# Optimization experiments

Hardware: AMD Instinct MI355X
Metric: run time of the kernel (lower is better)

Reference implementation:

```python
import jax, jax.numpy as jnp
import numpy as np
jax.config.update("jax_enable_x64", True)  # RWKV6 uses fp64 intra-chunk decay when chunk_len > 24

B, T, D, H = 2, 2048, 2048, 32
K = D // H
CHUNK = 128
EPS = 1e-5 * 8 ** 2  # GroupNorm eps * head_size_divisor**2


def setup_inputs() -> dict:
    ks = jax.random.split(jax.random.key(0), 24)
    f32 = jnp.float32
    s = 1.0 / np.sqrt(D).astype(np.float32)
    u = lambda k, sh, lo, hi: jax.random.uniform(k, sh, f32, lo, hi)
    n = lambda k, sh, sc=1.0: jax.random.normal(k, sh, f32) * sc
    return {
        "x": n(ks[0], (B, T, D)),
        "shift_state": n(ks[1], (B, D)),
        "wkv_state": jnp.zeros((B, H, K, K), f32),
        "time_maa_x": u(ks[2], (1, 1, D), 0.0, 1.0),
        "time_maa_w": u(ks[3], (1, 1, D), 0.0, 1.0),
        "time_maa_k": u(ks[4], (1, 1, D), 0.0, 1.0),
        "time_maa_v": u(ks[5], (1, 1, D), 0.0, 1.0),
        "time_maa_r": u(ks[6], (1, 1, D), 0.0, 1.0),
        "time_maa_g": u(ks[7], (1, 1, D), 0.0, 1.0),
        "time_maa_w1": n(ks[8], (D, 32 * 5), 0.01),
        "time_maa_w2": u(ks[9], (5, 32, D), -0.01, 0.01),
        "time_decay": u(ks[10], (1, 1, D), -6.0, -1.0),
        "time_decay_w1": n(ks[11], (D, 64), 0.1),
        "time_decay_w2": u(ks[12], (64, D), -0.01, 0.01),
        "time_faaaa": u(ks[13], (H, K), -0.1, 1.0),
        "W_r": n(ks[14], (D, D), s),
        "W_k": n(ks[15], (D, D), s),
        "W_v": n(ks[16], (D, D), s),
        "W_g": n(ks[17], (D, D), s),
        "W_o": n(ks[18], (D, D), s),
        "ln_gamma": jnp.ones((D,), f32),
        "ln_beta": jnp.zeros((D,), f32),
    }


def _wkv_chunked(r, k, v, w, u, state):
    """RWKV6 WKV: parallel intra-chunk (chunk_len=128, fp64 decay) + scan over chunks."""
    Bq, Hq, L, Kq = r.shape
    Tc = CHUNK
    N = L // Tc
    w_decay = jnp.clip(jnp.exp(w), 0.005, None)
    w_log = jnp.log(w_decay.astype(jnp.float32))
    wc_log = w_log.reshape(Bq, Hq, N, Tc, Kq)
    wc_cum = jnp.cumsum(wc_log, axis=-2)                               # (B,H,N,T,K)
    shifted = jnp.pad(wc_cum, ((0, 0),) * 3 + ((1, 0), (0, 0)))[..., :Tc, :]
    ws = jnp.sum(wc_log, axis=-2, keepdims=True)                        # (B,H,N,1,K)
    w_inter = jnp.exp(ws - wc_cum).astype(r.dtype)
    w_intra = jnp.exp(wc_cum - wc_log).astype(r.dtype)
    rc = r.reshape(Bq, Hq, N, Tc, Kq)
    kc = k.reshape(Bq, Hq, N, Tc, Kq)
    vc = v.reshape(Bq, Hq, N, Tc, Kq)
    off = shifted[..., Tc // 2:Tc // 2 + 1, :]
    r_decay = jnp.exp((shifted - off).astype(jnp.float64))
    k_inv = jnp.exp((off - wc_cum).astype(jnp.float64))
    a = jnp.einsum('bhnik,bhnjk->bhnij', rc * r_decay, kc * k_inv).astype(r.dtype)
    a = jnp.tril(a, -1)
    diag = jnp.einsum('bhntk,bhntk->bhnt', rc, u[:, :, None] * kc)      # u bonus on diagonal
    a = a + diag[..., None] * jnp.eye(Tc, dtype=a.dtype)
    out = jnp.einsum('bhnij,bhnjv->bhniv', a, vc)
    wkv = jnp.einsum('bhntk,bhntv->bhnkv', kc * w_inter, vc)
    ws_e = jnp.exp(ws)[..., 0, :, None].astype(r.dtype)                 # (B,H,N,K,1)

    def step(s, xs):
        wkv_i, ws_i = xs
        return s * ws_i + wkv_i, s  # emit state BEFORE update

    final, states = jax.lax.scan(step, state, (jnp.moveaxis(wkv, 2, 0), jnp.moveaxis(ws_e, 2, 0)))
    states = jnp.moveaxis(states, 0, 2)                                 # (B,H,N,K,V)
    out = out + jnp.einsum('bhntk,bhnkv->bhntv', rc * w_intra, states)
    return out.reshape(Bq, Hq, L, Kq), final


def _group_norm(x, n_groups, gamma, beta, eps):
    Bq, Tq, Dq = x.shape
    xg = x.reshape(Bq, Tq, n_groups, Dq // n_groups)
    mu = jnp.mean(xg, axis=-1, keepdims=True)
    var = jnp.var(xg, axis=-1, keepdims=True)
    xn = ((xg - mu) / jnp.sqrt(var + eps)).reshape(Bq, Tq, Dq)
    return xn * gamma + beta


def reference(x, shift_state, wkv_state, time_maa_x, time_maa_w, time_maa_k, time_maa_v,
              time_maa_r, time_maa_g, time_maa_w1, time_maa_w2, time_decay, time_decay_w1,
              time_decay_w2, time_faaaa, W_r, W_k, W_v, W_g, W_o, ln_gamma, ln_beta):
    Bq, Tq, Dq = x.shape
    Hq = time_faaaa.shape[0]
    Kq = Dq // Hq
    dxprev = jnp.concatenate([shift_state[:, None], x[:, :-1]], axis=1) - x
    xxx = x + dxprev * time_maa_x
    m = jnp.tanh(xxx @ time_maa_w1).reshape(Bq, Tq, 5, -1)
    m = jnp.einsum('btfm,fmd->fbtd', m, time_maa_w2)
    mw, mk, mv, mr, mg = m[0], m[1], m[2], m[3], m[4]
    xw = x + dxprev * (time_maa_w + mw)
    xk = x + dxprev * (time_maa_k + mk)
    xv = x + dxprev * (time_maa_v + mv)
    xr = x + dxprev * (time_maa_r + mr)
    xg = x + dxprev * (time_maa_g + mg)
    r = xr @ W_r.T
    k = xk @ W_k.T
    v = xv @ W_v.T
    g = jax.nn.silu(xg @ W_g.T)
    w = time_decay + jnp.tanh(xw @ time_decay_w1) @ time_decay_w2
    heads = lambda t: t.reshape(Bq, Tq, Hq, Kq).transpose(0, 2, 1, 3)
    r, k, v = heads(r), heads(k), heads(v)
    w = -jnp.exp(heads(w))
    u = time_faaaa.reshape(1, Hq, 1, Kq)
    x_out, wkv_out = _wkv_chunked(r, k, v, w, u, wkv_state)
    x_out = x_out.transpose(0, 2, 1, 3).reshape(Bq, Tq, Dq)
    x_out = _group_norm(x_out, Hq, ln_gamma, ln_beta, EPS)
    out = (x_out * g) @ W_o.T
    return out, x[:, -1], wkv_out
```

## Files before the change

kernel.cpp:

```cpp
#include <hip/hip_runtime.h>

#define B_ 2
#define T_ 2048
#define D_ 2048
#define H_ 32
#define BT_ 4096
#define TC 128

typedef unsigned short u16;
typedef unsigned int u32;
typedef __attribute__((ext_vector_type(8))) short short8;
typedef __attribute__((ext_vector_type(4))) float floatx4;

__device__ __forceinline__ float bf2f(u16 u){ return __uint_as_float(((u32)u)<<16); }
__device__ __forceinline__ u16 f2bf(float f){
  u32 i = __float_as_uint(f);
  if ((i & 0x7F800000u) == 0x7F800000u) return 0;
  return (u16)((i + 0x7FFFu + ((i>>16)&1u)) >> 16);
}
__device__ __forceinline__ float ldf(const void* p, int f, size_t i){
  return f ? ((const float*)p)[i] : bf2f(((const u16*)p)[i]);
}
__device__ __forceinline__ void async16(const u16* g, u16* l){
  __builtin_amdgcn_global_load_lds((const __attribute__((address_space(1))) void*)g,
                                   (__attribute__((address_space(3))) void*)l, 16, 0, 0);
}
__device__ __forceinline__ float sexp(float x){ return expf(fminf(x, 85.f)); }

#define LN005 -5.2983173665480363f

struct DetArgs { const void* p[22]; int n[22]; };

__global__ void k_detect(DetArgs a, int* fl){
  int t = threadIdx.x;
  if (t < 22){
    int bad = 0;
    if (t == 20){
      u32 w = *(const u32*)a.p[t];
      bad = (w == 0x3F800000u) ? 1 : 0;
    } else {
      int n = a.n[t];
      int step = n/256; if (step < 1) step = 1;
      const u16* u = (const u16*)a.p[t];
      for (int s=0; s<128; ++s){
        int j = (s*step) & ~1;
        if (j < n){
          u32 e = ((u32)u[j] >> 7) & 0xFFu;
          if (e >= 0xC0u) bad = 1;
        }
      }
    }
    fl[t] = bad;
  }
  __syncthreads();
  if (t == 0) fl[22] = fl[0];
}

__global__ void k_zero(u16* o, int n){
  int i = blockIdx.x*256 + threadIdx.x;
  if (i < n) o[i] = 0;
}

__global__ void k_wcvt(const void* __restrict__ src, const int* __restrict__ fl, int fidx,
                       u16* __restrict__ dst)
{
  if (!fl[fidx]) return;
  size_t i = ((size_t)blockIdx.x*256 + threadIdx.x)*8;
  const float* s = (const float*)src + i;
  float4 a0 = *(const float4*)s, a1 = *(const float4*)(s+4);
  u16 t[8] = {f2bf(a0.x),f2bf(a0.y),f2bf(a0.z),f2bf(a0.w),
              f2bf(a1.x),f2bf(a1.y),f2bf(a1.z),f2bf(a1.w)};
  *(uint4*)(dst + i) = *(uint4*)t;
}

__global__ void k_wtrans(const void* __restrict__ src, const int* __restrict__ fl, int fidx,
                         int K, int Nsrc, u16* __restrict__ dst)
{
  int f = fl[fidx];
  int kg = K >> 3;
  int i = blockIdx.x*256 + threadIdx.x;
  int n = i / kg, k0 = (i - n*kg) << 3;
  u16 tmp[8];
  if (n < Nsrc){
    if (f){
      const float* s = (const float*)src;
      #pragma unroll
      for (int j=0;j<8;++j) tmp[j] = f2bf(s[(size_t)(k0+j)*Nsrc + n]);
    } else {
      const u16* s = (const u16*)src;
      #pragma unroll
      for (int j=0;j<8;++j) tmp[j] = s[(size_t)(k0+j)*Nsrc + n];
    }
  } else {
    #pragma unroll
    for (int j=0;j<8;++j) tmp[j] = 0;
  }
  *(uint4*)(dst + (size_t)i*8) = *(uint4*)tmp;
}

__global__ void k_prep(const void* __restrict__ x, const void* __restrict__ shift,
                       const void* __restrict__ maax, const int* __restrict__ fl,
                       u16* __restrict__ dxp, u16* __restrict__ xxx)
{
  int xF = fl[0], sF = fl[1], mF = fl[3];
  int row = blockIdx.x;
  int t = row & (T_-1); int b = row >> 11;
  int d = threadIdx.x*8;
  size_t e = (size_t)row*D_ + d;
  float xf[8], pf[8], mf[8];
  if (xF){
    const float* xp = (const float*)x;
    float4 a0 = *(const float4*)(xp+e), a1 = *(const float4*)(xp+e+4);
    xf[0]=a0.x;xf[1]=a0.y;xf[2]=a0.z;xf[3]=a0.w;xf[4]=a1.x;xf[5]=a1.y;xf[6]=a1.z;xf[7]=a1.w;
    if (t>0){
      float4 p0 = *(const float4*)(xp+e-D_), p1 = *(const float4*)(xp+e-D_+4);
      pf[0]=p0.x;pf[1]=p0.y;pf[2]=p0.z;pf[3]=p0.w;pf[4]=p1.x;pf[5]=p1.y;pf[6]=p1.z;pf[7]=p1.w;
    } else {
      #pragma unroll
      for (int j=0;j<8;++j) pf[j] = ldf(shift, sF, (size_t)b*D_ + d + j);
    }
  } else {
    const u16* xp = (const u16*)x;
    u16 tmp[8];
    *(uint4*)tmp = *(const uint4*)(xp+e);
    #pragma unroll
    for (int j=0;j<8;++j) xf[j]=bf2f(tmp[j]);
    if (t>0){
      *(uint4*)tmp = *(const uint4*)(xp+e-D_);
      #pragma unroll
      for (int j=0;j<8;++j) pf[j]=bf2f(tmp[j]);
    } else {
      #pragma unroll
      for (int j=0;j<8;++j) pf[j] = ldf(shift, sF, (size_t)b*D_ + d + j);
    }
  }
  if (mF){
    const float* mp = (const float*)maax;
    float4 m0 = *(const float4*)(mp+d), m1 = *(const float4*)(mp+d+4);
    mf[0]=m0.x;mf[1]=m0.y;mf[2]=m0.z;mf[3]=m0.w;mf[4]=m1.x;mf[5]=m1.y;mf[6]=m1.z;mf[7]=m1.w;
  } else {
    #pragma unroll
    for (int j=0;j<8;++j) mf[j] = bf2f(((const u16*)maax)[d+j]);
  }
  u16 od[8], ox[8];
  #pragma unroll
  for (int j=0;j<8;++j){
    float dx = pf[j]-xf[j];
    od[j]=f2bf(dx);
    ox[j]=f2bf(xf[j]+dx*mf[j]);
  }
  *(uint4*)(dxp+e) = *(uint4*)od;
  *(uint4*)(xxx+e) = *(uint4*)ox;
}

#define EPI_BF16 0
#define EPI_OUT  1
#define EPI_TANH 2
#define EPI_WLOG 3
#define EPI_V    4
__global__ __launch_bounds__(256) void k_gemm(
    const u16* __restrict__ A, const void* __restrict__ Bsrc, const u16* __restrict__ Bcvt,
    void* __restrict__ Cv,
    int N, int K, int lda, int ldb,
    const int* __restrict__ fl, int bFlagIdx, int epi,
    const void* __restrict__ bias, int biasFlagIdx)
{
  __shared__ u16 As[128*64];
  __shared__ u16 Bs[128*64];
  const u16* Bp = ((bFlagIdx >= 0) && fl[bFlagIdx]) ? Bcvt : (const u16*)Bsrc;
  int tid = threadIdx.x;
  int wave = tid>>6, lane = tid&63;
  int q = lane>>4, l15 = lane&15;
  int row0 = blockIdx.x*128, col0 = blockIdx.y*128;
  int wm = (wave&1)*64, wn = (wave>>1)*64;
  floatx4 acc[4][4];
  #pragma unroll
  for (int i=0;i<4;++i)
    #pragma unroll
    for (int j=0;j<4;++j) acc[i][j] = (floatx4){0.f,0.f,0.f,0.f};

  for (int k0=0;k0<K;k0+=64){
    #pragma unroll
    for (int r=0;r<4;++r){
      int s = r*256 + tid;
      int row = s>>3, c8 = s&7;
      async16(A  + (size_t)(row0+row)*lda + k0 + c8*8, &As[s*8]);
      async16(Bp + (size_t)(col0+row)*ldb + k0 + c8*8, &Bs[s*8]);
    }
    __syncthreads();
    #pragma unroll
    for (int ks=0;ks<2;++ks){
      short8 af[4], bfv[4];
      #pragma unroll
      for (int i=0;i<4;++i){
        af[i]  = *(const short8*)&As[(wm + i*16 + l15)*64 + (ks*4+q)*8];
        bfv[i] = *(const short8*)&Bs[(wn + i*16 + l15)*64 + (ks*4+q)*8];
      }
      #pragma unroll
      for (int i=0;i<4;++i)
        #pragma unroll
        for (int j=0;j<4;++j)
          acc[i][j] = __builtin_amdgcn_mfma_f32_16x16x32_bf16(af[i], bfv[j], acc[i][j], 0,0,0);
    }
    __syncthreads();
  }
  if (epi == EPI_V){
    #pragma unroll
    for (int i=0;i<4;++i)
      #pragma unroll
      for (int j=0;j<4;++j){
        int row = row0 + wm + i*16 + q*4;
        int col = col0 + wn + j*16 + l15;
        int bb = row>>11, ta = row&2047;
        int nn = ta>>7, tt = ta&127;
        int h2 = col>>6, dim = col&63;
        u16 pk[4];
        #pragma unroll
        for (int rr=0;rr<4;++rr) pk[rr] = f2bf(acc[i][j][rr]);
        size_t vidx = ((size_t)(bb*H_+h2)*16+nn)*8192 + (size_t)dim*128 + tt;
        *(uint2*)((u16*)Cv + vidx) = *(uint2*)pk;
      }
    return;
  }
  int biasF = (biasFlagIdx >= 0) ? fl[biasFlagIdx] : 0;
  int oF = fl[22];
  #pragma unroll
  for (int i=0;i<4;++i)
    #pragma unroll
    for (int j=0;j<4;++j)
      #pragma unroll
      for (int rr=0;rr<4;++rr){
        int row = row0 + wm + i*16 + q*4 + rr;
        int col = col0 + wn + j*16 + l15;
        size_t idx = (size_t)row*N + col;
        float v = acc[i][j][rr];
        if (epi == EPI_BF16){
          ((u16*)Cv)[idx] = f2bf(v);
        } else if (epi == EPI_TANH){
          ((u16*)Cv)[idx] = f2bf(tanhf(v));
        } else if (epi == EPI_WLOG){
          float a = v + ldf(bias, biasF, col);
          a = fminf(a, 0.f);
          ((float*)Cv)[idx] = fmaxf(-expf(a), LN005);
        } else {
          if (oF) ((float*)Cv)[idx] = v;
          else    ((u16*)Cv)[idx] = f2bf(v);
        }
      }
}

__global__ __launch_bounds__(256) void k_mix2(
    const void* __restrict__ x, const u16* __restrict__ dxp,
    const u16* __restrict__ mt, const void* __restrict__ w2,
    const void* __restrict__ mw, const void* __restrict__ mk2,
    const void* __restrict__ mv, const void* __restrict__ mr,
    const void* __restrict__ mg, const int* __restrict__ fl,
    u16* __restrict__ xw, u16* __restrict__ xk, u16* __restrict__ xv,
    u16* __restrict__ xr, u16* __restrict__ xg)
{
  __shared__ u16 w2s[128][162];
  __shared__ u16 mts[160][64];
  int tid = threadIdx.x;
  int d0 = blockIdx.x*128, r0 = blockIdx.y*64;
  int xF = fl[0], wF = fl[10];
  if (wF){
    const float* wp = (const float*)w2;
    for (int i=tid; i<160*128; i+=256){
      int fm = i>>7, dc = i&127;
      w2s[dc][fm] = f2bf(wp[(size_t)fm*2048 + d0+dc]);
    }
  } else {
    const u16* wp = (const u16*)w2;
    for (int i=tid; i<160*128; i+=256){
      int fm = i>>7, dc = i&127;
      w2s[dc][fm] = wp[(size_t)fm*2048 + d0+dc];
    }
  }
  for (int i=tid; i<160*64; i+=256){
    int c = i>>6, r = i&63;
    mts[c][r] = mt[(size_t)(r0+r)*256 + c];
  }
  __syncthreads();
  int tdl = tid&31, tr = tid>>5;
  int rbase = tr*8;
  float xfv[4][8], dfv[4][8];
  if (xF){
    const float* xp = (const float*)x;
    #pragma unroll
    for (int dd=0; dd<4; ++dd){
      int d = d0 + tdl + 32*dd;
      #pragma unroll
      for (int rr=0; rr<8; ++rr){
        size_t e = (size_t)(r0+rbase+rr)*D_ + d;
        xfv[dd][rr] = xp[e];
        dfv[dd][rr] = bf2f(dxp[e]);
      }
    }
  } else {
    const u16* xp = (const u16*)x;
    #pragma unroll
    for (int dd=0; dd<4; ++dd){
      int d = d0 + tdl + 32*dd;
      #pragma unroll
      for (int rr=0; rr<8; ++rr){
        size_t e = (size_t)(r0+rbase+rr)*D_ + d;
        xfv[dd][rr] = bf2f(xp[e]);
        dfv[dd][rr] = bf2f(dxp[e]);
      }
    }
  }
  const void* maas[5] = {mw,mk2,mv,mr,mg};
  const int mfl[5] = {fl[4],fl[5],fl[6],fl[7],fl[8]};
  u16* outs[5] = {xw,xk,xv,xr,xg};
  #pragma unroll
  for (int f=0; f<5; ++f){
    float acc[4][8];
    #pragma unroll
    for (int dd=0;dd<4;++dd)
      #pragma unroll
      for (int rr=0;rr<8;++rr) acc[dd][rr]=0.f;
    for (int m=0; m<32; ++m){
      int fm = f*32+m;
      float wv[4];
      #pragma unroll
      for (int dd=0;dd<4;++dd) wv[dd] = bf2f(w2s[tdl+32*dd][fm]);
      short8 m8 = *(const short8*)&mts[fm][rbase];
      #pragma unroll
      for (int rr=0;rr<8;++rr){
        float mvf = bf2f((u16)m8[rr]);
        #pragma unroll
        for (int dd=0;dd<4;++dd) acc[dd][rr] += wv[dd]*mvf;
      }
    }
    float basev[4];
    #pragma unroll
    for (int dd=0;dd<4;++dd) basev[dd] = ldf(maas[f], mfl[f], d0 + tdl + 32*dd);
    u16* op = outs[f];
    #pragma unroll
    for (int dd=0;dd<4;++dd){
      int d = d0 + tdl + 32*dd;
      #pragma unroll
      for (int rr=0;rr<8;++rr){
        size_t e = (size_t)(r0+rbase+rr)*D_ + d;
        op[e] = f2bf(xfv[dd][rr] + dfv[dd][rr]*(basev[dd] + acc[dd][rr]));
      }
    }
  }
}

__global__ void k_wkv1(const u16* __restrict__ kk, const u16* __restrict__ vbT,
                       const float* __restrict__ wlog, u16* __restrict__ wkvT, float* __restrict__ wse)
{
  __shared__ u16 kt[128][64];
  __shared__ __align__(16) u16 vsT[64*128];
  __shared__ float segs[4][64];
  __shared__ float wsk[64];
  int tid=threadIdx.x, lane=tid&63, seg=tid>>6;
  int bx=blockIdx.x; int n=bx&15, hh=(bx>>4)&31, b=bx>>9;
  size_t base = ((size_t)(b*T_ + n*TC))*D_ + (size_t)hh*64;
  size_t cbase = ((size_t)(b*H_+hh)*16+n)*8192;
  #pragma unroll
  for (int it=0; it<4; ++it){
    int s = it*256 + tid;
    async16(vbT + cbase + (size_t)s*8, &vsT[s*8]);
  }
  float s=0.f;
  for (int t0=0;t0<32;++t0) s += wlog[base + (size_t)(seg*32+t0)*D_ + lane];
  segs[seg][lane]=s;
  __syncthreads();
  if (seg==0){
    float tot=segs[0][lane]+segs[1][lane]+segs[2][lane]+segs[3][lane];
    wsk[lane]=tot; wse[(size_t)bx*64+lane]=expf(tot);
  }
  __syncthreads();
  float run=0.f;
  for (int ss=0;ss<seg;++ss) run += segs[ss][lane];
  float wst = wsk[lane];
  for (int t0=0;t0<32;++t0){
    int t = seg*32+t0;
    size_t gi = base + (size_t)t*D_ + lane;
    run += wlog[gi];
    kt[t][lane] = f2bf(bf2f(kk[gi]) * sexp(wst - run));
  }
  __syncthreads();
  float acc[16];
  #pragma unroll
  for (int i=0;i<16;++i) acc[i]=0.f;
  for (int t=0;t<128;++t){
    float kf = bf2f(kt[t][lane]);
    #pragma unroll
    for (int vi=0;vi<16;++vi) acc[vi] += kf * bf2f(vsT[(seg*16+vi)*128 + t]);
  }
  u16* op = wkvT + (size_t)bx*4096;
  #pragma unroll
  for (int vi=0;vi<16;++vi) op[(seg*16+vi)*64 + lane] = f2bf(acc[vi]);
}

__global__ void k_scan(const u16* __restrict__ wkvT, const float* __restrict__ wse,
                       const void* __restrict__ st0, const int* __restrict__ fl,
                       u16* __restrict__ stpre, float* __restrict__ finT)
{
  int fs = fl[2];
  int tid=threadIdx.x; int bh=blockIdx.x;
  int kidx = tid&63;
  float S[16];
  #pragma unroll
  for (int i=0;i<16;++i){
    int e = tid + 256*i; int vvv = e>>6; int kk2 = e&63;
    S[i] = ldf(st0, fs, (size_t)bh*4096 + kk2*64 + vvv);
  }
  for (int n=0;n<16;++n){
    size_t cb = ((size_t)bh*16+n)*4096;
    float wsv = wse[((size_t)bh*16+n)*64 + kidx];
    #pragma unroll
    for (int i=0;i<16;++i){
      int e = tid + 256*i;
      stpre[cb+e] = f2bf(S[i]);
      S[i] = S[i]*wsv + bf2f(wkvT[cb+e]);
    }
  }
  #pragma unroll
  for (int i=0;i<16;++i){
    float v = S[i];
    if (!(v==v)) v = 0.f;
    finT[(size_t)bh*4096 + tid + 256*i] = v;
  }
}

__global__ __launch_bounds__(512) void k_wkv2(
    const u16* __restrict__ rg, const u16* __restrict__ kk, const u16* __restrict__ vbT,
    const float* __restrict__ wlog, const u16* __restrict__ stpre, const void* __restrict__ faaaa,
    const int* __restrict__ fl, u16* __restrict__ xo)
{
  __shared__ __align__(16) u16 RA[128*64];
  __shared__ __align__(16) u16 KSB[128*128];
  __shared__ __align__(16) u16 VT[64*128];
  __shared__ __align__(16) u16 STB[64*64];
  __shared__ float segsw[8][64];
  __shared__ float diag[128];
  __shared__ float fv[64];

  int ff = fl[14];
  int tid=threadIdx.x, lane=tid&63, seg=tid>>6;
  int q = lane>>4, l15 = lane&15;
  int bx=blockIdx.x; int n=bx&15, hh=(bx>>4)&31, b=bx>>9;
  size_t base = ((size_t)(b*T_ + n*TC))*D_ + (size_t)hh*64;
  size_t cbase = ((size_t)(b*H_+hh)*16+n)*8192;

  #pragma unroll
  for (int it=0; it<2; ++it){
    int s = it*512 + tid;
    async16(vbT + cbase + (size_t)s*8, &VT[s*8]);
  }

  float s=0.f;
  for (int t0=0;t0<16;++t0) s += wlog[base + (size_t)(seg*16+t0)*D_ + lane];
  segsw[seg][lane]=s;
  __syncthreads();
  float off=0.f, run=0.f;
  #pragma unroll
  for (int ss=0;ss<4;++ss) off += segsw[ss][lane];
  for (int ss=0;ss<seg;++ss) run += segsw[ss][lane];
  if (seg==0) fv[lane]=expf(off);
  float uf = ldf(faaaa, ff, hh*64+lane);
  for (int t0=0;t0<16;++t0){
    int t = seg*16+t0;
    size_t gi = base + (size_t)t*D_ + lane;
    float wl = wlog[gi];
    float wcx = run; run += wl;
    float rf = bf2f(rg[gi]);
    float kf = bf2f(kk[gi]);
    RA[t*64+lane]  = f2bf(rf * sexp(wcx - off));
    KSB[t*64+lane] = f2bf(kf * sexp(off - run));
    float dv = rf*uf*kf;
    #pragma unroll
    for (int o2=32;o2;o2>>=1) dv += __shfl_xor(dv, o2, 64);
    if (lane==0) diag[t]=dv;
  }
  __syncthreads();

  {
    int s4 = tid*8;
    const u16* sp = stpre + (size_t)bx*4096 + s4;
    u16 in[8]; *(uint4*)in = *(const uint4*)sp;
    int k0 = s4 & 63;
    u16 ot[8];
    #pragma unroll
    for (int j=0;j<8;++j) ot[j] = f2bf(bf2f(in[j]) * fv[k0+j]);
    *(uint4*)&STB[s4] = *(uint4*)ot;
  }

  int wm_ = (seg&1)*64, wn_ = (seg>>1)*32;
  floatx4 sa[4][2];
  #pragma unroll
  for (int i=0;i<4;++i){ sa[i][0]=(floatx4){0,0,0,0}; sa[i][1]=(floatx4){0,0,0,0}; }
  #pragma unroll
  for (int ks=0;ks<2;++ks){
    short8 af[4], bfv[2];
    #pragma unroll
    for (int i=0;i<4;++i) af[i] = *(const short8*)&RA[(wm_+i*16+l15)*64 + ks*32 + q*8];
    #pragma unroll
    for (int j=0;j<2;++j) bfv[j] = *(const short8*)&KSB[(wn_+j*16+l15)*64 + ks*32 + q*8];
    #pragma unroll
    for (int i=0;i<4;++i)
      #pragma unroll
      for (int j=0;j<2;++j)
        sa[i][j] = __builtin_amdgcn_mfma_f32_16x16x32_bf16(af[i], bfv[j], sa[i][j], 0,0,0);
  }
  __syncthreads();

  #pragma unroll
  for (int i=0;i<4;++i)
    #pragma unroll
    for (int j=0;j<2;++j)
      #pragma unroll
      for (int rr=0;rr<4;++rr){
        int gi_ = wm_ + i*16 + q*4 + rr;
        int gj  = wn_ + j*16 + l15;
        KSB[gi_*128 + gj] = (gj < gi_) ? f2bf(sa[i][j][rr]) : (u16)0;
      }
  __syncthreads();

  int rw = seg&1, cw = seg>>1;
  floatx4 o2[4];
  #pragma unroll
  for (int i=0;i<4;++i) o2[i]=(floatx4){0,0,0,0};
  #pragma unroll
  for (int k4=0;k4<4;++k4){
    short8 bfv = *(const short8*)&VT[(cw*16+l15)*128 + k4*32 + q*8];
    #pragma unroll
    for (int i=0;i<4;++i){
      short8 af = *(const short8*)&KSB[(rw*64+i*16+l15)*128 + k4*32 + q*8];
      o2[i] = __builtin_amdgcn_mfma_f32_16x16x32_bf16(af, bfv, o2[i], 0,0,0);
    }
  }
  #pragma unroll
  for (int ks=0;ks<2;++ks){
    short8 bfv = *(const short8*)&STB[(cw*16+l15)*64 + ks*32 + q*8];
    #pragma unroll
    for (int i=0;i<4;++i){
      short8 af = *(const short8*)&RA[(rw*64+i*16+l15)*64 + ks*32 + q*8];
      o2[i] = __builtin_amdgcn_mfma_f32_16x16x32_bf16(af, bfv, o2[i], 0,0,0);
    }
  }
  #pragma unroll
  for (int i=0;i<4;++i)
    #pragma unroll
    for (int rr=0;rr<4;++rr){
      int gi_ = rw*64 + i*16 + q*4 + rr;
      int gv  = cw*16 + l15;
      float acc = o2[i][rr] + diag[gi_]*bf2f(VT[gv*128 + gi_]);
      xo[base + (size_t)gi_*D_ + gv] = f2bf(acc);
    }
}

__global__ void k_gnorm(const u16* __restrict__ xo, const u16* __restrict__ glin,
                        const void* __restrict__ gamma, const void* __restrict__ beta,
                        const int* __restrict__ fl, u16* __restrict__ y)
{
  int fg = fl[20], fb = fl[21];
  int tid=threadIdx.x; int wv=tid>>6, lane=tid&63;
  int g = blockIdx.x*4 + wv;
  int bt = g>>5, hh = g&31;
  size_t e = (size_t)bt*D_ + hh*64 + lane;
  float v = bf2f(xo[e]);
  float s1 = v, s2 = v*v;
  #pragma unroll
  for (int o=32;o;o>>=1){ s1 += __shfl_xor(s1,o,64); s2 += __shfl_xor(s2,o,64); }
  float mean = s1*(1.0f/64.0f);
  float var = s2*(1.0f/64.0f) - mean*mean;
  float rstd = rsqrtf(fmaxf(var, 0.f) + 6.4e-4f);
  float xn = (v-mean)*rstd;
  xn = xn*ldf(gamma, fg, hh*64+lane) + ldf(beta, fb, hh*64+lane);
  float gv = bf2f(glin[e]);
  float sig = 1.0f/(1.0f + expf(-gv));
  y[e] = f2bf(xn * gv * sig);
}

__global__ void k_outs(const void* __restrict__ x, const float* __restrict__ finT,
                       const int* __restrict__ fl, void* __restrict__ dout)
{
  int xF = fl[0], oF = fl[22];
  int i = blockIdx.x*256 + threadIdx.x;
  if (i < 4096){
    int b = i>>11, d = i&2047;
    float v = ldf(x, xF, ((size_t)b*T_ + (T_-1))*D_ + d);
    size_t oi = 8388608 + (size_t)i;
    if (oF) ((float*)dout)[oi] = v; else ((u16*)dout)[oi] = f2bf(v);
  } else {
    int j = i - 4096;
    int vv2 = j&63, kk2=(j>>6)&63, bh=j>>12;
    float v = finT[(size_t)bh*4096 + vv2*64 + kk2];
    size_t oi = 8392704 + (size_t)j;
    if (oF) ((float*)dout)[oi] = v; else ((u16*)dout)[oi] = f2bf(v);
  }
}

extern "C" void kernel_launch(void* const* d_in, const int* in_sizes, int n_in,
                              void* d_out, int out_size, void* d_ws, size_t ws_size,
                              hipStream_t stream)
{
  (void)n_in;
  const size_t NEED = 512ull + 120061952ull;
  if (ws_size < NEED){
    k_zero<<<(out_size+255)/256,256,0,stream>>>((u16*)d_out, out_size);
    return;
  }

  int* fl = (int*)d_ws;
  char* ws = (char*)d_ws + 512;

  DetArgs da;
  for (int i=0;i<22;++i){ da.p[i] = d_in[i]; da.n[i] = in_sizes[i]; }
  k_detect<<<1,64,0,stream>>>(da, fl);

  const void* x      = d_in[0];
  const void* shift  = d_in[1];
  const void* state0 = d_in[2];
  const void* maax   = d_in[3];
  const void* maaw   = d_in[4];
  const void* maak   = d_in[5];
  const void* maav   = d_in[6];
  const void* maar   = d_in[7];
  const void* maag   = d_in[8];
  const void* w1     = d_in[9];
  const void* w2     = d_in[10];
  const void* tdec   = d_in[11];
  const void* dw1    = d_in[12];
  const void* dw2    = d_in[13];
  const void* faaaa  = d_in[14];
  const void* Wr     = d_in[15];
  const void* Wk     = d_in[16];
  const void* Wv     = d_in[17];
  const void* Wg     = d_in[18];
  const void* Wo     = d_in[19];
  const void* gamma  = d_in[20];
  const void* beta   = d_in[21];

  u16*  dxp  = (u16*)(ws + 0);
  u16*  xxx  = (u16*)(ws + 16777216);
  float* wlog= (float*)(ws + 0);
  u16*  WoB  = (u16*)(ws + 0);
  u16*  xw   = (u16*)(ws + 33554432);
  u16*  rb   = (u16*)(ws + 33554432);
  u16*  y    = (u16*)(ws + 33554432);
  u16*  xk   = (u16*)(ws + 50331648);
  u16*  vbT  = (u16*)(ws + 50331648);
  u16*  xv   = (u16*)(ws + 67108864);
  u16*  gl   = (u16*)(ws + 67108864);
  u16*  xr   = (u16*)(ws + 83886080);
  u16*  kb   = (u16*)(ws + 83886080);
  u16*  xg   = (u16*)(ws + 100663296);
  u16*  wkvT = (u16*)(ws + 100663296);
  u16*  stpre= (u16*)(ws + 109051904);
  u16*  mt   = (u16*)(ws + 117440512);
  u16*  hb   = (u16*)(ws + 117440512);
  float* finT= (float*)(ws + 117440512);
  float* wse = (float*)(ws + 119537664);
  u16*  xout = (u16*)d_out;
  u16*  Wb   = (u16*)d_out;
  u16*  P1   = (u16*)d_out + 4194304;

  k_prep<<<4096,256,0,stream>>>(x, shift, maax, fl, dxp, xxx);
  k_wtrans<<<256,256,0,stream>>>(w1, fl, 9, 2048, 160, P1);
  k_gemm<<<dim3(32,2),256,0,stream>>>(xxx, P1, P1, mt, 256, 2048, 2048, 2048,
                                      fl, -1, EPI_TANH, nullptr, -1);
  k_mix2<<<dim3(16,64),256,0,stream>>>(x, dxp, mt, w2, maaw,maak,maav,maar,maag, fl, xw,xk,xv,xr,xg);
  k_wtrans<<<128,256,0,stream>>>(dw1, fl, 12, 2048, 64, P1);
  k_gemm<<<dim3(32,1),256,0,stream>>>(xw, P1, P1, hb, 128, 2048, 2048, 2048,
                                      fl, -1, EPI_TANH, nullptr, -1);
  k_wtrans<<<64,256,0,stream>>>(dw2, fl, 13, 64, 2048, P1);
  k_gemm<<<dim3(32,16),256,0,stream>>>(hb, P1, P1, wlog, 2048, 64, 128, 64,
                                      fl, -1, EPI_WLOG, tdec, 11);
  k_wcvt<<<2048,256,0,stream>>>(Wr, fl, 15, Wb);
  k_gemm<<<dim3(32,16),256,0,stream>>>(xr, Wr, Wb, rb, 2048, 2048, 2048, 2048,
                                      fl, 15, EPI_BF16, nullptr, -1);
  k_wcvt<<<2048,256,0,stream>>>(Wk, fl, 16, Wb);
  k_gemm<<<dim3(32,16),256,0,stream>>>(xk, Wk, Wb, kb, 2048, 2048, 2048, 2048,
                                      fl, 16, EPI_BF16, nullptr, -1);
  k_wcvt<<<2048,256,0,stream>>>(Wv, fl, 17, Wb);
  k_gemm<<<dim3(32,16),256,0,stream>>>(xv, Wv, Wb, vbT, 2048, 2048, 2048, 2048,
                                      fl, 17, EPI_V, nullptr, -1);
  k_wcvt<<<2048,256,0,stream>>>(Wg, fl, 18, Wb);
  k_gemm<<<dim3(32,16),256,0,stream>>>(xg, Wg, Wb, gl, 2048, 2048, 2048, 2048,
                                      fl, 18, EPI_BF16, nullptr, -1);
  k_wkv1<<<1024,256,0,stream>>>(kb, vbT, wlog, wkvT, wse);
  k_scan<<<64,256,0,stream>>>(wkvT, wse, state0, fl, stpre, finT);
  k_wkv2<<<1024,512,0,stream>>>(rb, kb, vbT, wlog, stpre, faaaa, fl, xout);
  k_wcvt<<<2048,256,0,stream>>>(Wo, fl, 19, WoB);
  k_gnorm<<<32768,256,0,stream>>>(xout, gl, gamma, beta, fl, y);
  k_gemm<<<dim3(32,16),256,0,stream>>>(y, Wo, WoB, d_out, 2048, 2048, 2048, 2048,
                                      fl, 19, EPI_OUT, nullptr, -1);
  k_outs<<<1040,256,0,stream>>>(x, finT, fl, d_out);
}
```

Measured before the change: 912.3 us.

## Compute token-shift mix projections with bf16 MFMA instead of scalar FMA

Replaces the scalar-FMA k_mix2 kernel, which staged w2 and the tanh activations in shared memory, with k_mix3. The new kernel reads them straight from global memory and computes each of the five 32-wide projections with one 16x16x32 bf16 MFMA per output tile. A k_wtrans launch first transposes w2 into bf16 so the per-lane B fragments can be loaded as contiguous 8-element vectors. This cuts the ALU work of the mix stage. In exchange it adds an extra transpose launch and re-reads x and dxp once per projection in the MFMA output layout, which is only partly coalesced (16 columns per row).

```diff
diff --git a/kernel.cpp b/kernel.cpp
--- a/kernel.cpp
+++ b/kernel.cpp
@@ -249,102 +249,57 @@
       }
 }
 
-__global__ __launch_bounds__(256) void k_mix2(
+__global__ __launch_bounds__(256) void k_mix3(
     const void* __restrict__ x, const u16* __restrict__ dxp,
-    const u16* __restrict__ mt, const void* __restrict__ w2,
+    const u16* __restrict__ mt, const u16* __restrict__ w2T,
     const void* __restrict__ mw, const void* __restrict__ mk2,
     const void* __restrict__ mv, const void* __restrict__ mr,
     const void* __restrict__ mg, const int* __restrict__ fl,
     u16* __restrict__ xw, u16* __restrict__ xk, u16* __restrict__ xv,
     u16* __restrict__ xr, u16* __restrict__ xg)
 {
-  __shared__ u16 w2s[128][162];
-  __shared__ u16 mts[160][64];
   int tid = threadIdx.x;
-  int d0 = blockIdx.x*128, r0 = blockIdx.y*64;
-  int xF = fl[0], wF = fl[10];
-  if (wF){
-    const float* wp = (const float*)w2;
-    for (int i=tid; i<160*128; i+=256){
-      int fm = i>>7, dc = i&127;
-      w2s[dc][fm] = f2bf(wp[(size_t)fm*2048 + d0+dc]);
-    }
-  } else {
-    const u16* wp = (const u16*)w2;
-    for (int i=tid; i<160*128; i+=256){
-      int fm = i>>7, dc = i&127;
-      w2s[dc][fm] = wp[(size_t)fm*2048 + d0+dc];
-    }
-  }
-  for (int i=tid; i<160*64; i+=256){
-    int c = i>>6, r = i&63;
-    mts[c][r] = mt[(size_t)(r0+r)*256 + c];
-  }
-  __syncthreads();
-  int tdl = tid&31, tr = tid>>5;
-  int rbase = tr*8;
-  float xfv[4][8], dfv[4][8];
-  if (xF){
-    const float* xp = (const float*)x;
-    #pragma unroll
-    for (int dd=0; dd<4; ++dd){
-      int d = d0 + tdl + 32*dd;
-      #pragma unroll
-      for (int rr=0; rr<8; ++rr){
-        size_t e = (size_t)(r0+rbase+rr)*D_ + d;
-        xfv[dd][rr] = xp[e];
-        dfv[dd][rr] = bf2f(dxp[e]);
-      }
-    }
-  } else {
-    const u16* xp = (const u16*)x;
-    #pragma unroll
-    for (int dd=0; dd<4; ++dd){
-      int d = d0 + tdl + 32*dd;
-      #pragma unroll
-      for (int rr=0; rr<8; ++rr){
-        size_t e = (size_t)(r0+rbase+rr)*D_ + d;
-        xfv[dd][rr] = bf2f(xp[e]);
-        dfv[dd][rr] = bf2f(dxp[e]);
-      }
-    }
-  }
+  int wave = tid>>6, lane = tid&63;
+  int q = lane>>4, l15 = lane&15;
+  int row0 = blockIdx.x*128, col0 = blockIdx.y*128;
+  int wm = (wave&1)*64, wn = (wave>>1)*64;
+  int xF = fl[0];
   const void* maas[5] = {mw,mk2,mv,mr,mg};
   const int mfl[5] = {fl[4],fl[5],fl[6],fl[7],fl[8]};
   u16* outs[5] = {xw,xk,xv,xr,xg};
   #pragma unroll
   for (int f=0; f<5; ++f){
-    float acc[4][8];
-    #pragma unroll
-    for (int dd=0;dd<4;++dd)
-      #pragma unroll
-      for (int rr=0;rr<8;++rr) acc[dd][rr]=0.f;
-    for (int m=0; m<32; ++m){
-      int fm = f*32+m;
-      float wv[4];
-      #pragma unroll
-      for (int dd=0;dd<4;++dd) wv[dd] = bf2f(w2s[tdl+32*dd][fm]);
-      short8 m8 = *(const short8*)&mts[fm][rbase];
-      #pragma unroll
-      for (int rr=0;rr<8;++rr){
-        float mvf = bf2f((u16)m8[rr]);
+    short8 af[4], bfv[4];
+    #pragma unroll
+    for (int i=0;i<4;++i)
+      af[i]  = *(const short8*)&mt[(size_t)(row0+wm+i*16+l15)*256 + f*32 + q*8];
+    #pragma unroll
+    for (int j=0;j<4;++j)
+      bfv[j] = *(const short8*)&w2T[(size_t)(col0+wn+j*16+l15)*160 + f*32 + q*8];
+    floatx4 acc[4][4];
+    #pragma unroll
+    for (int i=0;i<4;++i)
+      #pragma unroll
+      for (int j=0;j<4;++j)
+        acc[i][j] = __builtin_amdgcn_mfma_f32_16x16x32_bf16(af[i], bfv[j],
+                      (floatx4){0.f,0.f,0.f,0.f}, 0,0,0);
+    float maav_[4];
+    #pragma unroll
+    for (int j=0;j<4;++j) maav_[j] = ldf(maas[f], mfl[f], col0 + wn + j*16 + l15);
+    u16* op = outs[f];
+    #pragma unroll
+    for (int i=0;i<4;++i)
+      #pragma unroll
+      for (int j=0;j<4;++j)
         #pragma unroll
-        for (int dd=0;dd<4;++dd) acc[dd][rr] += wv[dd]*mvf;
-      }
-    }
-    float basev[4];
-    #pragma unroll
-    for (int dd=0;dd<4;++dd) basev[dd] = ldf(maas[f], mfl[f], d0 + tdl + 32*dd);
-    u16* op = outs[f];
-    #pragma unroll
-    for (int dd=0;dd<4;++dd){
-      int d = d0 + tdl + 32*dd;
-      #pragma unroll
-      for (int rr=0;rr<8;++rr){
-        size_t e = (size_t)(r0+rbase+rr)*D_ + d;
-        op[e] = f2bf(xfv[dd][rr] + dfv[dd][rr]*(basev[dd] + acc[dd][rr]));
-      }
-    }
+        for (int rr=0;rr<4;++rr){
+          int row = row0 + wm + i*16 + q*4 + rr;
+          int col = col0 + wn + j*16 + l15;
+          size_t e = (size_t)row*D_ + col;
+          float xfv = xF ? ((const float*)x)[e] : bf2f(((const u16*)x)[e]);
+          float dfv = bf2f(dxp[e]);
+          op[e] = f2bf(xfv + dfv*(maav_[j] + acc[i][j][rr]));
+        }
   }
 }
 
@@ -665,7 +620,9 @@
   k_wtrans<<<256,256,0,stream>>>(w1, fl, 9, 2048, 160, P1);
   k_gemm<<<dim3(32,2),256,0,stream>>>(xxx, P1, P1, mt, 256, 2048, 2048, 2048,
                                       fl, -1, EPI_TANH, nullptr, -1);
-  k_mix2<<<dim3(16,64),256,0,stream>>>(x, dxp, mt, w2, maaw,maak,maav,maar,maag, fl, xw,xk,xv,xr,xg);
+  k_wtrans<<<160,256,0,stream>>>(w2, fl, 10, 160, 2048, P1);
+  k_mix3<<<dim3(32,16),256,0,stream>>>(x, dxp, mt, P1, maaw,maak,maav,maar,maag, fl,
+                                       xw,xk,xv,xr,xg);
   k_wtrans<<<128,256,0,stream>>>(dw1, fl, 12, 2048, 64, P1);
   k_gemm<<<dim3(32,1),256,0,stream>>>(xw, P1, P1, hb, 128, 2048, 2048, 2048,
                                       fl, -1, EPI_TANH, nullptr, -1);
```

New measurement: 943.3 us. 1.03x slower.
